# Kernel optimization log

Hardware: AMD Instinct MI355X
Metric: run time of the kernel (lower is better)

Reference implementation:

```python
import jax, jax.numpy as jnp
import numpy as np

T = 2048          # total (flattened) tokens
HID = 4096
NQ = 32           # query heads
NKV = 8           # kv heads
D = 128           # head_dim
B = 4             # dllm block length (block-sparse attention block)
WIN = 1024        # sliding window
EPS = 1e-6


def _rope_tables():
    # standard RoPE cos/sin tables, half-dim frequencies duplicated
    inv_freq = 1.0 / (10000.0 ** (np.arange(0, D, 2, dtype=np.float32) / D))
    pos = np.arange(T, dtype=np.float32)
    freqs = np.outer(pos, inv_freq)                     # [T, D/2]
    emb = np.concatenate([freqs, freqs], axis=-1)       # [T, D]
    return jnp.asarray(np.cos(emb)), jnp.asarray(np.sin(emb))


def setup_inputs() -> dict:
    key = jax.random.key(0)
    ks = jax.random.split(key, 4)
    cos, sin = _rope_tables()
    return {
        "hidden_states": jax.random.normal(ks[0], (T, HID), jnp.float32),
        "cos": cos,
        "sin": sin,
        "w_qkv": jax.random.normal(ks[1], (HID, (NQ + 2 * NKV) * D), jnp.float32) * (HID ** -0.5),
        "q_norm_w": jnp.ones((D,), jnp.float32),
        "k_norm_w": jnp.ones((D,), jnp.float32),
        "w_o": jax.random.normal(ks[2], (NQ * D, HID), jnp.float32) * ((NQ * D) ** -0.5),
    }


def _rmsnorm(x, w):
    # per-head RMSNorm over last dim (head_dim)
    var = jnp.mean(jnp.square(x), axis=-1, keepdims=True)
    return x * jax.lax.rsqrt(var + EPS) * w


def _rotate_half(x):
    x1, x2 = jnp.split(x, 2, axis=-1)
    return jnp.concatenate([-x2, x1], axis=-1)


def reference(hidden_states, cos, sin, w_qkv, q_norm_w, k_norm_w, w_o):
    # fused QKV projection on flattened tokens [T, HID]
    qkv = hidden_states @ w_qkv                                  # [T, (NQ+2NKV)*D]
    q, k, v = jnp.split(qkv, [NQ * D, (NQ + NKV) * D], axis=-1)
    q = q.reshape(T, NQ, D)
    k = k.reshape(T, NKV, D)
    v = v.reshape(T, NKV, D)

    # per-head QK RMSNorm
    q = _rmsnorm(q, q_norm_w)
    k = _rmsnorm(k, k_norm_w)

    # RoPE
    c = cos[:, None, :]
    s = sin[:, None, :]
    q = q * c + _rotate_half(q) * s
    k = k * c + _rotate_half(k) * s

    # GQA: expand kv heads to query heads
    groups = NQ // NKV
    k = jnp.repeat(k, groups, axis=1)                            # [T, NQ, D]
    v = jnp.repeat(v, groups, axis=1)

    # block-sparse (dLLM block-causal) + sliding-window mask:
    # token q attends to token j iff block(j) <= block(q) (full bidirectional
    # attention within a dllm block, causal across blocks) AND j is within
    # the sliding window.
    pos = jnp.arange(T)
    qb = pos // B
    allowed = (qb[None, :] <= qb[:, None]) & ((pos[:, None] - pos[None, :]) < WIN)

    scale = D ** -0.5
    scores = jnp.einsum("qhd,khd->hqk", q, k) * scale            # [NQ, T, T]
    scores = jnp.where(allowed[None, :, :], scores, jnp.float32(-1e30))
    probs = jax.nn.softmax(scores, axis=-1)
    attn = jnp.einsum("hqk,khd->qhd", probs, v)                   # [T, NQ, D]

    out = attn.reshape(T, NQ * D) @ w_o                           # [T, HID]
    return out
```

## Files before the change

### kernel.cpp

```cpp
#include <hip/hip_runtime.h>
#include <hip/hip_bf16.h>

typedef unsigned short u16;
typedef __attribute__((ext_vector_type(8))) short bf16x8;
typedef __attribute__((ext_vector_type(4))) float f32x4;
typedef __attribute__((ext_vector_type(8))) u16 u16x8;
typedef __attribute__((ext_vector_type(4))) u16 u16x4;

#define T_SEQ 2048
#define HID 4096
#define NQ 32
#define NKV 8
#define DH 128
#define WIN 1024

__device__ __forceinline__ u16 f2bf(float f) {
  union { float f; unsigned int u; } v; v.f = f;
  unsigned int u = v.u;
  unsigned int r = (u + 0x7FFFu + ((u >> 16) & 1u)) >> 16;
  return (u16)r;
}
__device__ __forceinline__ float bf2f(u16 b) {
  union { unsigned int u; float f; } v; v.u = ((unsigned int)b) << 16;
  return v.f;
}

__device__ __forceinline__ void gload16(const void* g, void* l) {
  __builtin_amdgcn_global_load_lds(
      (const __attribute__((address_space(1))) unsigned int*)g,
      (__attribute__((address_space(3))) unsigned int*)l, 16, 0, 0);
}

__global__ __launch_bounds__(256) void f32_to_bf16(const float* __restrict__ in,
                                                   u16* __restrict__ out, int n) {
  int i = (blockIdx.x * 256 + threadIdx.x) * 8;
  if (i >= n) return;
  float4 a = *(const float4*)(in + i);
  float4 b = *(const float4*)(in + i + 4);
  u16x8 r;
  r[0] = f2bf(a.x); r[1] = f2bf(a.y); r[2] = f2bf(a.z); r[3] = f2bf(a.w);
  r[4] = f2bf(b.x); r[5] = f2bf(b.y); r[6] = f2bf(b.z); r[7] = f2bf(b.w);
  *(u16x8*)(out + i) = r;
}

__global__ __launch_bounds__(256) void transpose_f32_to_bf16(const float* __restrict__ in,
                                                             u16* __restrict__ out,
                                                             int R, int C) {
  __shared__ float tile[32][33];
  int c0 = blockIdx.x * 32, r0 = blockIdx.y * 32;
  int tx = threadIdx.x, ty = threadIdx.y;
  for (int i = 0; i < 32; i += 8)
    tile[ty + i][tx] = in[(size_t)(r0 + ty + i) * C + c0 + tx];
  __syncthreads();
  for (int i = 0; i < 32; i += 8)
    out[(size_t)(c0 + ty + i) * R + r0 + tx] = f2bf(tile[tx][ty + i]);
}

template <int NF, bool BF16OUT>
__global__ __launch_bounds__(512, 2) void gemm_np(const u16* __restrict__ A,
                                                  const u16* __restrict__ Bt,
                                                  void* __restrict__ Cv,
                                                  int N, int K, int NT) {
  constexpr int HN = NF * 16;
  constexpr int BN = 4 * HN;
  constexpr int NB = BN / 64;
  __shared__ u16 lsA[2][16384];
  __shared__ u16 lsB[2][BN * 64];
  const int tid = threadIdx.x;
  const int lane = tid & 63, w = tid >> 6;
  const int wm = w >> 1, wn = w & 1;
  const int l15 = lane & 15, l4 = lane >> 4;

  const int nwg = gridDim.x;
  const int cpx = nwg >> 3;
  const int bid = blockIdx.x;
  const int swz = (bid & 7) * cpx + (bid >> 3);
  const int bm = (swz & 7) * 256;
  const int bn = (swz >> 3) * BN;

  auto stageA = [&](int unit, int slot, int kt) {
    int r = tid >> 3, cp = tid & 7;
    int scp = cp ^ (r & 7);
    gload16(A + (size_t)(bm + unit * 64 + r) * K + kt * 64 + scp * 8,
            (char*)lsA[slot] + (unit * 512 + tid) * 16);
  };
  auto stageB = [&](int unit, int slot, int kt) {
    int r = tid >> 3, cp = tid & 7;
    int scp = cp ^ (r & 7);
    gload16(Bt + (size_t)(bn + unit * 64 + r) * K + kt * 64 + scp * 8,
            (char*)lsB[slot] + (unit * 512 + tid) * 16);
  };
  auto rdA = [&](int slot, int mh, int mf, int ks) -> bf16x8 {
    int r = wm * 64 + mh * 32 + mf * 16 + l15;
    int ch = (ks * 4 + l4) ^ (r & 7);
    return *(const bf16x8*)(lsA[slot] + r * 64 + ch * 8);
  };
  auto rdB = [&](int slot, int nh, int nf, int ks) -> bf16x8 {
    int r = wn * 2 * HN + nh * HN + nf * 16 + l15;
    int ch = (ks * 4 + l4) ^ (r & 7);
    return *(const bf16x8*)(lsB[slot] + r * 64 + ch * 8);
  };

#define WAIT_NB() do { if constexpr (NB == 3) asm volatile("s_waitcnt vmcnt(3)" ::: "memory"); \
                       else                   asm volatile("s_waitcnt vmcnt(2)" ::: "memory"); } while (0)

  f32x4 acc[4][2 * NF] = {};
  bf16x8 afA[2][2], afB[2][2], bfr0[NF][2], bfr1[NF][2];

  stageA(0, 0, 0); stageA(1, 0, 0); stageA(2, 0, 0); stageA(3, 0, 0);
#pragma unroll
  for (int u = 0; u < NB; ++u) stageB(u, 0, 0);
#pragma unroll
  for (int u = 0; u < NB; ++u) stageB(u, 1, 1);
  WAIT_NB();
  __builtin_amdgcn_s_barrier();

  for (int t = 0; t < NT; ++t) {
    const int s = t & 1;
    const int ktA = (t + 1 < NT) ? t + 1 : NT - 1;
    const int ktB = (t + 2 < NT) ? t + 2 : NT - 1;

#pragma unroll
    for (int mf = 0; mf < 2; ++mf)
#pragma unroll
      for (int ks = 0; ks < 2; ++ks) afA[mf][ks] = rdA(s, 0, mf, ks);
#pragma unroll
    for (int nf = 0; nf < NF; ++nf)
#pragma unroll
      for (int ks = 0; ks < 2; ++ks) bfr0[nf][ks] = rdB(s, 0, nf, ks);
    stageA(0, s ^ 1, ktA); stageA(1, s ^ 1, ktA);
    __builtin_amdgcn_s_barrier();
    asm volatile("s_waitcnt lgkmcnt(0)" ::: "memory");
    __builtin_amdgcn_sched_barrier(0);
    __builtin_amdgcn_s_setprio(1);
#pragma unroll
    for (int mf = 0; mf < 2; ++mf)
#pragma unroll
      for (int nf = 0; nf < NF; ++nf) {
        acc[mf][nf] = __builtin_amdgcn_mfma_f32_16x16x32_bf16(afA[mf][0], bfr0[nf][0], acc[mf][nf], 0, 0, 0);
        acc[mf][nf] = __builtin_amdgcn_mfma_f32_16x16x32_bf16(afA[mf][1], bfr0[nf][1], acc[mf][nf], 0, 0, 0);
      }
    __builtin_amdgcn_s_setprio(0);
    __builtin_amdgcn_s_barrier();

#pragma unroll
    for (int nf = 0; nf < NF; ++nf)
#pragma unroll
      for (int ks = 0; ks < 2; ++ks) bfr1[nf][ks] = rdB(s, 1, nf, ks);
    stageA(2, s ^ 1, ktA); stageA(3, s ^ 1, ktA);
    __builtin_amdgcn_s_barrier();
    asm volatile("s_waitcnt lgkmcnt(0)" ::: "memory");
    __builtin_amdgcn_sched_barrier(0);
    __builtin_amdgcn_s_setprio(1);
#pragma unroll
    for (int mf = 0; mf < 2; ++mf)
#pragma unroll
      for (int nf = 0; nf < NF; ++nf) {
        acc[mf][NF + nf] = __builtin_amdgcn_mfma_f32_16x16x32_bf16(afA[mf][0], bfr1[nf][0], acc[mf][NF + nf], 0, 0, 0);
        acc[mf][NF + nf] = __builtin_amdgcn_mfma_f32_16x16x32_bf16(afA[mf][1], bfr1[nf][1], acc[mf][NF + nf], 0, 0, 0);
      }
    __builtin_amdgcn_s_setprio(0);
    __builtin_amdgcn_s_barrier();

#pragma unroll
    for (int mf = 0; mf < 2; ++mf)
#pragma unroll
      for (int ks = 0; ks < 2; ++ks) afB[mf][ks] = rdA(s, 1, mf, ks);
#pragma unroll
    for (int u = 0; u < NB - 1; ++u) stageB(u, s, ktB);
    __builtin_amdgcn_s_barrier();
    asm volatile("s_waitcnt lgkmcnt(0)" ::: "memory");
    __builtin_amdgcn_sched_barrier(0);
    __builtin_amdgcn_s_setprio(1);
#pragma unroll
    for (int mf = 0; mf < 2; ++mf)
#pragma unroll
      for (int nf = 0; nf < NF; ++nf) {
        acc[2 + mf][nf] = __builtin_amdgcn_mfma_f32_16x16x32_bf16(afB[mf][0], bfr0[nf][0], acc[2 + mf][nf], 0, 0, 0);
        acc[2 + mf][nf] = __builtin_amdgcn_mfma_f32_16x16x32_bf16(afB[mf][1], bfr0[nf][1], acc[2 + mf][nf], 0, 0, 0);
      }
    __builtin_amdgcn_s_setprio(0);
    __builtin_amdgcn_s_barrier();

    stageB(NB - 1, s, ktB);
    __builtin_amdgcn_s_barrier();
    __builtin_amdgcn_s_setprio(1);
#pragma unroll
    for (int mf = 0; mf < 2; ++mf)
#pragma unroll
      for (int nf = 0; nf < NF; ++nf) {
        acc[2 + mf][NF + nf] = __builtin_amdgcn_mfma_f32_16x16x32_bf16(afB[mf][0], bfr1[nf][0], acc[2 + mf][NF + nf], 0, 0, 0);
        acc[2 + mf][NF + nf] = __builtin_amdgcn_mfma_f32_16x16x32_bf16(afB[mf][1], bfr1[nf][1], acc[2 + mf][NF + nf], 0, 0, 0);
      }
    __builtin_amdgcn_s_setprio(0);
    WAIT_NB();
    __builtin_amdgcn_s_barrier();
  }

  asm volatile("s_waitcnt vmcnt(0)" ::: "memory");

#pragma unroll
  for (int mi = 0; mi < 4; ++mi)
#pragma unroll
    for (int ni = 0; ni < 2 * NF; ++ni) {
      int row = bm + wm * 64 + mi * 16 + l4 * 4;
      int col = bn + wn * 2 * HN + ni * 16 + l15;
      if constexpr (BF16OUT) {
        u16* dst = (u16*)Cv;
#pragma unroll
        for (int j = 0; j < 4; ++j)
          dst[(size_t)(row + j) * N + col] = f2bf(acc[mi][ni][j]);
      } else {
        float* p = (float*)Cv + (size_t)row * N + col;
        p[0] = acc[mi][ni][0];
        p[(size_t)N] = acc[mi][ni][1];
        p[2 * (size_t)N] = acc[mi][ni][2];
        p[3 * (size_t)N] = acc[mi][ni][3];
      }
    }
#undef WAIT_NB
}

__global__ __launch_bounds__(256) void rope_kernel(const u16* __restrict__ qkv,
                                                   const float* __restrict__ cosb,
                                                   const float* __restrict__ sinb,
                                                   const float* __restrict__ qw,
                                                   const float* __restrict__ kw,
                                                   u16* __restrict__ Qo,
                                                   u16* __restrict__ Ko,
                                                   u16* __restrict__ Vt) {
  int wid = threadIdx.x >> 6, lane = threadIdx.x & 63;
  int item = blockIdx.x * 4 + wid;
  int t = item / 48, hid = item % 48;
  const u16* x = qkv + (size_t)t * 6144 + hid * 128;
  float x1 = bf2f(x[lane]), x2 = bf2f(x[lane + 64]);
  if (hid < NQ + NKV) {
    float ss = x1 * x1 + x2 * x2;
    for (int off = 32; off; off >>= 1) ss += __shfl_xor(ss, off);
    float inv = rsqrtf(ss * (1.0f / 128.0f) + 1e-6f);
    const float* wn = (hid < NQ) ? qw : kw;
    float n1 = x1 * inv * wn[lane], n2 = x2 * inv * wn[lane + 64];
    float c1 = cosb[t * 128 + lane], s1 = sinb[t * 128 + lane];
    float c2 = cosb[t * 128 + lane + 64], s2 = sinb[t * 128 + lane + 64];
    float o1 = n1 * c1 - n2 * s1;
    float o2 = n2 * c2 + n1 * s2;
    if (hid < NQ) {
      const float scale = 0.08838834764831845f;
      u16* q = Qo + ((size_t)hid * T_SEQ + t) * 128;
      q[lane] = f2bf(o1 * scale); q[lane + 64] = f2bf(o2 * scale);
    } else {
      int h = hid - NQ;
      u16* k = Ko + ((size_t)h * T_SEQ + t) * 128;
      k[lane] = f2bf(o1); k[lane + 64] = f2bf(o2);
    }
  } else {
    int h = hid - (NQ + NKV);
    Vt[((size_t)h * 128 + lane) * T_SEQ + t] = x[lane];
    Vt[((size_t)h * 128 + lane + 64) * T_SEQ + t] = x[lane + 64];
  }
}

__global__ __launch_bounds__(256) void attn_kernel(const u16* __restrict__ Q,
                                                   const u16* __restrict__ Kb,
                                                   const u16* __restrict__ Vt,
                                                   u16* __restrict__ O) {
  __shared__ u16 kls[2][64 * 128];
  __shared__ u16 vls[2][128 * 64];
  __shared__ u16 plds[4][16 * 72];

  const int tid = threadIdx.x;
  const int lane = tid & 63, w = tid >> 6;
  const int l15 = lane & 15, l4 = lane >> 4;
  const int h = blockIdx.x;
  const int q0 = blockIdx.y * 64;
  const int wq0 = q0 + w * 16;
  const int kvh = h >> 2;

  bf16x8 qf[4];
  {
    const u16* qrow = Q + ((size_t)h * T_SEQ + (wq0 + l15)) * DH;
    for (int ks = 0; ks < 4; ++ks)
      qf[ks] = *(const bf16x8*)(qrow + ks * 32 + l4 * 8);
  }

  f32x4 acc[8] = {};
  float m = -1e30f, lsum = 0.f;

  int ks0 = q0 - (WIN - 1); if (ks0 < 0) ks0 = 0;
  ks0 &= ~63;
  const int kend = q0;

  auto stage = [&](int b, int k0) {
#pragma unroll
    for (int c = 0; c < 4; ++c) {
      int base = w * 4096 + c * 1024;
      int idx = base / 16 + lane;
      {
        int row = idx >> 4;
        int col = (idx & 15) ^ (row & 7);
        gload16(Kb + ((size_t)kvh * T_SEQ + k0 + row) * DH + col * 8,
                (char*)kls[b] + base);
      }
      {
        int d = idx >> 3;
        int ch = (idx & 7) ^ (d & 7);
        gload16(Vt + ((size_t)kvh * DH + d) * T_SEQ + k0 + ch * 8,
                (char*)vls[b] + base);
      }
    }
  };

  stage(0, ks0);
  int buf = 0;
  for (int k0 = ks0; k0 <= kend; k0 += 64) {
    bool more = (k0 + 64 <= kend);
    if (more) stage(buf ^ 1, k0 + 64);
    if (more) { asm volatile("s_waitcnt vmcnt(8)" ::: "memory"); }
    else      { asm volatile("s_waitcnt vmcnt(0)" ::: "memory"); }
    __builtin_amdgcn_s_barrier();
    __builtin_amdgcn_sched_barrier(0);

    if (k0 <= wq0 + 15 && k0 + 63 >= wq0 - (WIN - 1)) {
      f32x4 st[4];
#pragma unroll
      for (int kh = 0; kh < 4; ++kh) {
        f32x4 s = {};
        int row = kh * 16 + l15;
        const char* kb = (const char*)kls[buf] + row * 256;
#pragma unroll
        for (int ks = 0; ks < 4; ++ks) {
          int chunk = (ks * 4 + l4) ^ (row & 7);
          bf16x8 kf = *(const bf16x8*)(kb + chunk * 16);
          s = __builtin_amdgcn_mfma_f32_16x16x32_bf16(kf, qf[ks], s, 0, 0, 0);
        }
        st[kh] = s;
      }
      const int q = wq0 + l15;
      float pv[4][4];
      float mx = -3e38f;
#pragma unroll
      for (int kh = 0; kh < 4; ++kh)
#pragma unroll
        for (int i = 0; i < 4; ++i) {
          int k = k0 + kh * 16 + l4 * 4 + i;
          bool ok = ((k >> 2) <= (q >> 2)) && (q - k < WIN);
          float s = ok ? st[kh][i] : -3e38f;
          pv[kh][i] = s;
          mx = fmaxf(mx, s);
        }
      mx = fmaxf(mx, __shfl_xor(mx, 16));
      mx = fmaxf(mx, __shfl_xor(mx, 32));
      if (!__all(mx <= m + 8.f)) {
        float mn = fmaxf(m, mx);
        float sc = __expf(m - mn);
        m = mn;
        lsum *= sc;
#pragma unroll
        for (int nt = 0; nt < 8; ++nt)
#pragma unroll
          for (int i = 0; i < 4; ++i) acc[nt][i] *= sc;
      }
      float rs = 0.f;
#pragma unroll
      for (int kh = 0; kh < 4; ++kh)
#pragma unroll
        for (int i = 0; i < 4; ++i) {
          float p = __expf(pv[kh][i] - m);
          pv[kh][i] = p;
          rs += p;
        }
      rs += __shfl_xor(rs, 16);
      rs += __shfl_xor(rs, 32);
      lsum += rs;
      u16* pw = plds[w];
#pragma unroll
      for (int kh = 0; kh < 4; ++kh) {
        unsigned int d0 = (unsigned int)f2bf(pv[kh][0]) | ((unsigned int)f2bf(pv[kh][1]) << 16);
        unsigned int d1 = (unsigned int)f2bf(pv[kh][2]) | ((unsigned int)f2bf(pv[kh][3]) << 16);
        *(unsigned int*)(pw + l15 * 72 + kh * 16 + l4 * 4) = d0;
        *(unsigned int*)(pw + l15 * 72 + kh * 16 + l4 * 4 + 2) = d1;
      }
      bf16x8 pf0 = *(const bf16x8*)(pw + l15 * 72 + l4 * 8);
      bf16x8 pf1 = *(const bf16x8*)(pw + l15 * 72 + 32 + l4 * 8);
#pragma unroll
      for (int nt = 0; nt < 8; ++nt) {
        int d = nt * 16 + l15;
        int ch0 = l4 ^ (d & 7);
        int ch1 = (4 + l4) ^ (d & 7);
        bf16x8 vf0 = *(const bf16x8*)((const char*)vls[buf] + d * 128 + ch0 * 16);
        bf16x8 vf1 = *(const bf16x8*)((const char*)vls[buf] + d * 128 + ch1 * 16);
        acc[nt] = __builtin_amdgcn_mfma_f32_16x16x32_bf16(vf0, pf0, acc[nt], 0, 0, 0);
        acc[nt] = __builtin_amdgcn_mfma_f32_16x16x32_bf16(vf1, pf1, acc[nt], 0, 0, 0);
      }
    }
    __builtin_amdgcn_sched_barrier(0);
    __builtin_amdgcn_s_barrier();
    buf ^= 1;
  }

  float inv = 1.0f / lsum;
#pragma unroll
  for (int nt = 0; nt < 8; ++nt) {
    u16x4 o;
#pragma unroll
    for (int i = 0; i < 4; ++i) o[i] = f2bf(acc[nt][i] * inv);
    *(u16x4*)(O + (size_t)(wq0 + l15) * (NQ * DH) + h * DH + nt * 16 + l4 * 4) = o;
  }
}

extern "C" void kernel_launch(void* const* d_in, const int* in_sizes, int n_in,
                              void* d_out, int out_size, void* d_ws, size_t ws_size,
                              hipStream_t stream) {
  const float* hidden = (const float*)d_in[0];
  const float* cosb   = (const float*)d_in[1];
  const float* sinb   = (const float*)d_in[2];
  const float* w_qkv  = (const float*)d_in[3];
  const float* qnw    = (const float*)d_in[4];
  const float* knw    = (const float*)d_in[5];
  const float* w_o    = (const float*)d_in[6];
  float* out = (float*)d_out;
  char* ws = (char*)d_ws;

  u16*   wqkvT  = (u16*)(ws);
  u16*   hid_bf = (u16*)(ws + ((size_t)48 << 20));
  u16*   qkv_bf = (u16*)(ws + ((size_t)64 << 20));
  u16*   q_bf   = (u16*)(ws + ((size_t)112 << 20));
  u16*   k_bf   = (u16*)(ws + ((size_t)128 << 20));
  u16*   vt_bf  = (u16*)(ws + ((size_t)132 << 20));
  u16*   attn_bf= (u16*)(ws + ((size_t)48 << 20));
  u16*   woT    = (u16*)(ws);

  f32_to_bf16<<<4096, 256, 0, stream>>>(hidden, hid_bf, T_SEQ * HID);
  transpose_f32_to_bf16<<<dim3(192, 128), dim3(32, 8), 0, stream>>>(w_qkv, wqkvT, HID, 6144);
  gemm_np<3, true><<<256, 512, 0, stream>>>(hid_bf, wqkvT, qkv_bf, 6144, HID, 64);
  transpose_f32_to_bf16<<<dim3(128, 128), dim3(32, 8), 0, stream>>>(w_o, woT, NQ * DH, HID);
  rope_kernel<<<(T_SEQ * 48) / 4, 256, 0, stream>>>(qkv_bf, cosb, sinb, qnw, knw, q_bf, k_bf, vt_bf);
  attn_kernel<<<dim3(NQ, T_SEQ / 64), 256, 0, stream>>>(q_bf, k_bf, vt_bf, attn_bf);
  gemm_np<2, false><<<256, 512, 0, stream>>>(attn_bf, woT, out, HID, NQ * DH, 64);
}
```

Baseline: 338.7 us.

## Process 128 queries per attention block with two 16-row tiles per wave

Each attention workgroup now handles 128 query rows instead of 64, with every wave holding two 16-row query tiles and separate softmax state and accumulators for each. K/V tiles staged in shared memory are reused across twice as many queries, roughly halving global K/V traffic and staging overhead per query. The cost is twice the accumulator registers per wave, which may lower occupancy, and half as many workgroups (512), which may leave compute units underfilled.

```diff
diff --git a/kernel.cpp b/kernel.cpp
--- a/kernel.cpp
+++ b/kernel.cpp
@@ -272,23 +272,25 @@
   const int lane = tid & 63, w = tid >> 6;
   const int l15 = lane & 15, l4 = lane >> 4;
   const int h = blockIdx.x;
-  const int q0 = blockIdx.y * 64;
-  const int wq0 = q0 + w * 16;
+  const int q0 = blockIdx.y * 128;
+  const int wq0 = q0 + w * 32;
   const int kvh = h >> 2;
 
-  bf16x8 qf[4];
-  {
-    const u16* qrow = Q + ((size_t)h * T_SEQ + (wq0 + l15)) * DH;
+  bf16x8 qf[2][4];
+#pragma unroll
+  for (int qh = 0; qh < 2; ++qh) {
+    const u16* qrow = Q + ((size_t)h * T_SEQ + (wq0 + qh * 16 + l15)) * DH;
+#pragma unroll
     for (int ks = 0; ks < 4; ++ks)
-      qf[ks] = *(const bf16x8*)(qrow + ks * 32 + l4 * 8);
+      qf[qh][ks] = *(const bf16x8*)(qrow + ks * 32 + l4 * 8);
   }
 
-  f32x4 acc[8] = {};
-  float m = -1e30f, lsum = 0.f;
+  f32x4 acc[2][8] = {};
+  float m[2] = {-1e30f, -1e30f}, lsum[2] = {0.f, 0.f};
 
   int ks0 = q0 - (WIN - 1); if (ks0 < 0) ks0 = 0;
   ks0 &= ~63;
-  const int kend = q0;
+  const int kend = q0 + 64;
 
   auto stage = [&](int b, int k0) {
 #pragma unroll
@@ -320,7 +322,11 @@
     __builtin_amdgcn_s_barrier();
     __builtin_amdgcn_sched_barrier(0);
 
-    if (k0 <= wq0 + 15 && k0 + 63 >= wq0 - (WIN - 1)) {
+#pragma unroll
+    for (int qh = 0; qh < 2; ++qh) {
+      const int wqq = wq0 + qh * 16;
+      if (k0 > wqq + 15 || k0 + 63 < wqq - (WIN - 1)) continue;
+
       f32x4 st[4];
 #pragma unroll
       for (int kh = 0; kh < 4; ++kh) {
@@ -331,11 +337,11 @@
         for (int ks = 0; ks < 4; ++ks) {
           int chunk = (ks * 4 + l4) ^ (row & 7);
           bf16x8 kf = *(const bf16x8*)(kb + chunk * 16);
-          s = __builtin_amdgcn_mfma_f32_16x16x32_bf16(kf, qf[ks], s, 0, 0, 0);
+          s = __builtin_amdgcn_mfma_f32_16x16x32_bf16(kf, qf[qh][ks], s, 0, 0, 0);
         }
         st[kh] = s;
       }
-      const int q = wq0 + l15;
+      const int q = wqq + l15;
       float pv[4][4];
       float mx = -3e38f;
 #pragma unroll
@@ -350,28 +356,28 @@
         }
       mx = fmaxf(mx, __shfl_xor(mx, 16));
       mx = fmaxf(mx, __shfl_xor(mx, 32));
-      if (!__all(mx <= m + 8.f)) {
-        float mn = fmaxf(m, mx);
-        float sc = __expf(m - mn);
-        m = mn;
-        lsum *= sc;
+      if (!__all(mx <= m[qh] + 8.f)) {
+        float mn = fmaxf(m[qh], mx);
+        float sc = __expf(m[qh] - mn);
+        m[qh] = mn;
+        lsum[qh] *= sc;
 #pragma unroll
         for (int nt = 0; nt < 8; ++nt)
 #pragma unroll
-          for (int i = 0; i < 4; ++i) acc[nt][i] *= sc;
+          for (int i = 0; i < 4; ++i) acc[qh][nt][i] *= sc;
       }
       float rs = 0.f;
 #pragma unroll
       for (int kh = 0; kh < 4; ++kh)
 #pragma unroll
         for (int i = 0; i < 4; ++i) {
-          float p = __expf(pv[kh][i] - m);
+          float p = __expf(pv[kh][i] - m[qh]);
           pv[kh][i] = p;
           rs += p;
         }
       rs += __shfl_xor(rs, 16);
       rs += __shfl_xor(rs, 32);
-      lsum += rs;
+      lsum[qh] += rs;
       u16* pw = plds[w];
 #pragma unroll
       for (int kh = 0; kh < 4; ++kh) {
@@ -389,8 +395,8 @@
         int ch1 = (4 + l4) ^ (d & 7);
         bf16x8 vf0 = *(const bf16x8*)((const char*)vls[buf] + d * 128 + ch0 * 16);
         bf16x8 vf1 = *(const bf16x8*)((const char*)vls[buf] + d * 128 + ch1 * 16);
-        acc[nt] = __builtin_amdgcn_mfma_f32_16x16x32_bf16(vf0, pf0, acc[nt], 0, 0, 0);
-        acc[nt] = __builtin_amdgcn_mfma_f32_16x16x32_bf16(vf1, pf1, acc[nt], 0, 0, 0);
+        acc[qh][nt] = __builtin_amdgcn_mfma_f32_16x16x32_bf16(vf0, pf0, acc[qh][nt], 0, 0, 0);
+        acc[qh][nt] = __builtin_amdgcn_mfma_f32_16x16x32_bf16(vf1, pf1, acc[qh][nt], 0, 0, 0);
       }
     }
     __builtin_amdgcn_sched_barrier(0);
@@ -398,13 +404,16 @@
     buf ^= 1;
   }
 
-  float inv = 1.0f / lsum;
-#pragma unroll
-  for (int nt = 0; nt < 8; ++nt) {
-    u16x4 o;
-#pragma unroll
-    for (int i = 0; i < 4; ++i) o[i] = f2bf(acc[nt][i] * inv);
-    *(u16x4*)(O + (size_t)(wq0 + l15) * (NQ * DH) + h * DH + nt * 16 + l4 * 4) = o;
+#pragma unroll
+  for (int qh = 0; qh < 2; ++qh) {
+    float inv = 1.0f / lsum[qh];
+#pragma unroll
+    for (int nt = 0; nt < 8; ++nt) {
+      u16x4 o;
+#pragma unroll
+      for (int i = 0; i < 4; ++i) o[i] = f2bf(acc[qh][nt][i] * inv);
+      *(u16x4*)(O + (size_t)(wq0 + qh * 16 + l15) * (NQ * DH) + h * DH + nt * 16 + l4 * 4) = o;
+    }
   }
 }
 
@@ -435,6 +444,6 @@
   gemm_np<3, true><<<256, 512, 0, stream>>>(hid_bf, wqkvT, qkv_bf, 6144, HID, 64);
   transpose_f32_to_bf16<<<dim3(128, 128), dim3(32, 8), 0, stream>>>(w_o, woT, NQ * DH, HID);
   rope_kernel<<<(T_SEQ * 48) / 4, 256, 0, stream>>>(qkv_bf, cosb, sinb, qnw, knw, q_bf, k_bf, vt_bf);
-  attn_kernel<<<dim3(NQ, T_SEQ / 64), 256, 0, stream>>>(q_bf, k_bf, vt_bf, attn_bf);
+  attn_kernel<<<dim3(NQ, T_SEQ / 128), 256, 0, stream>>>(q_bf, k_bf, vt_bf, attn_bf);
   gemm_np<2, false><<<256, 512, 0, stream>>>(attn_bf, woT, out, HID, NQ * DH, 64);
 }
```

Result: slower. 371.9 us (+9.8%).
